# Kernel tuning notes

Hardware: AMD Instinct MI355X
Metric: run time of the kernel (lower is better)

Reference implementation:

```python
import jax, jax.numpy as jnp
import numpy as np

_EPSILON = 1e-06
EPS = 0.05
MAX_ITER = 50
THRESHOLD = 0.001


def setup_inputs() -> dict:
    key = jax.random.key(0)
    k1, k2 = jax.random.split(key)
    source = jax.random.normal(k1, (8192, 64), dtype=jnp.float32)
    target = jax.random.normal(k2, (8192, 64), dtype=jnp.float32)
    return {"source": source, "target": target}


def _sinkhorn(source, target):
    source = source.astype(jnp.float32)
    target = target.astype(jnp.float32)
    # squared euclidean cost matrix [N, M] (cdist(p=2)**2)
    sq_s = jnp.sum(source * source, axis=1, keepdims=True)          # [N,1]
    sq_t = jnp.sum(target * target, axis=1, keepdims=True).T        # [1,M]
    cost = sq_s + sq_t - 2.0 * (source @ target.T)                  # [N,M]
    cost = jnp.maximum(cost, 0.0)

    n_source, n_target = cost.shape
    log_mu = jnp.full((n_source,), jnp.log(jnp.maximum(1.0 / n_source, _EPSILON)), dtype=jnp.float32)
    log_nu = jnp.full((n_target,), jnp.log(jnp.maximum(1.0 / n_target, _EPSILON)), dtype=jnp.float32)

    u0 = jnp.zeros((n_source,), dtype=jnp.float32)
    v0 = jnp.zeros((n_target,), dtype=jnp.float32)

    def step(carry, _):
        u, v, done = carry
        prev_u = u
        mc = (-cost + u[:, None] + v[None, :]) / EPS
        u_new = EPS * (log_mu - jax.nn.logsumexp(mc, axis=1)) + u
        mc2 = (-cost + u_new[:, None] + v[None, :]) / EPS
        v_new = EPS * (log_nu - jax.nn.logsumexp(mc2, axis=0)) + v
        # freeze state once converged (emulates the torch early break)
        u = jnp.where(done, u, u_new)
        v = jnp.where(done, v, v_new)
        done = done | (jnp.mean(jnp.abs(u_new - prev_u)) < THRESHOLD)
        return (u, v, done), None

    (u, v, _), _ = jax.lax.scan(step, (u0, v0, jnp.array(False)), None, length=MAX_ITER)

    transport_plan = jnp.exp((-cost + u[:, None] + v[None, :]) / EPS)
    return jnp.sum(transport_plan * cost)


def reference(source, target):
    return _sinkhorn(source, target)
```

## Files before the change

kernel.cpp:

```cpp
#include <hip/hip_runtime.h>

#define N      8192
#define KDIM   64
#define SCALE2     28.853900817779268f
#define INV_SCALE2 0.034657359027997264f
#define TWOSCALE   57.707801635558536f
#define EPSLN2     0.034657359027997264f
#define EPS_LOG_MU (-0.45054566736396444f)
#define THRESH     0.001f
#define NEG_BIG    (-1e30f)
#define NCHUNK  32
#define COLSPAN 256
#define NCT     16
#define NBUF    5
#define ROWS_PER_BLOCK 256

typedef __attribute__((ext_vector_type(8))) short bf16x8;
typedef __attribute__((ext_vector_type(4))) float f32x4;

static __device__ __forceinline__ float exp2fast(float x) { return __builtin_amdgcn_exp2f(x); }
static __device__ __forceinline__ float log2fast(float x) { return __builtin_amdgcn_logf(x); }

static __device__ __forceinline__ unsigned short f2bf(float f) {
    unsigned u = __float_as_uint(f);
    u += 0x7FFFu + ((u >> 16) & 1u);
    return (unsigned short)(u >> 16);
}
static __device__ __forceinline__ float bf2f(unsigned short h) {
    return __uint_as_float(((unsigned)h) << 16);
}

static __device__ __forceinline__ void load16_to_lds(const void* gptr, void* lptr) {
    __builtin_amdgcn_global_load_lds(
        (const __attribute__((address_space(1))) unsigned int*)gptr,
        (__attribute__((address_space(3))) unsigned int*)lptr,
        16, 0, 0);
}

static __device__ __forceinline__ void stage_tile(
        const unsigned short* __restrict__ CPhi, const unsigned short* __restrict__ CPlo,
        char* ldsbuf, int jb, int wave, int swz) {
    const char* gsrc = (const char*)(wave < 2 ? CPhi : CPlo);
    const char* g = gsrc + (size_t)jb * 128 + (size_t)((wave & 1) * 1024 + swz);
    char* l = ldsbuf + (wave & 1) * 1024 + (wave >> 1) * 2048;
    load16_to_lds(g, l);
}

static __device__ __forceinline__ void load_held(
        const unsigned short* __restrict__ RPhi, const unsigned short* __restrict__ RPlo,
        int rowbase, int lrow, int kgrp, bf16x8 (&bh)[4][2], bf16x8 (&bl)[4][2]) {
#pragma unroll
    for (int it = 0; it < 4; ++it)
#pragma unroll
        for (int ks = 0; ks < 2; ++ks) {
            int boff = (rowbase + it * 16 + lrow) * KDIM + ks * 32 + kgrp * 8;
            bh[it][ks] = *reinterpret_cast<const bf16x8*>(RPhi + boff);
            bl[it][ks] = *reinterpret_cast<const bf16x8*>(RPlo + boff);
            asm volatile("" : "+v"(bh[it][ks]));
            asm volatile("" : "+v"(bl[it][ks]));
        }
}

static __device__ __forceinline__ void barrier_lds_only() {
    asm volatile("s_waitcnt lgkmcnt(0)" ::: "memory");
    __builtin_amdgcn_sched_barrier(0);
    __builtin_amdgcn_s_barrier();
    __builtin_amdgcn_sched_barrier(0);
}

static __device__ __forceinline__ void pipe_wait(int n) {
    if (n >= 3)      asm volatile("s_waitcnt vmcnt(3)" ::: "memory");
    else if (n == 2) asm volatile("s_waitcnt vmcnt(2)" ::: "memory");
    else if (n == 1) asm volatile("s_waitcnt vmcnt(1)" ::: "memory");
    else             asm volatile("s_waitcnt vmcnt(0)" ::: "memory");
    __builtin_amdgcn_sched_barrier(0);
    __builtin_amdgcn_s_barrier();
    __builtin_amdgcn_sched_barrier(0);
}

static __device__ __forceinline__ void lse_loop(
        const unsigned short* __restrict__ CPhi, const unsigned short* __restrict__ CPlo,
        char* ldsA, const float* lds_alpha,
        const bf16x8 (&bh)[4][2], const bf16x8 (&bl)[4][2],
        int jbase0, int wave, int lane, int swz, float (&m)[4], float (&s)[4]) {
    const int lrow = lane & 15, kgrp = lane >> 4;
    const int ro = lrow * 128;
    const int x0 = ((kgrp)     ^ (lrow & 7)) * 16;
    const int x1 = ((kgrp + 4) ^ (lrow & 7)) * 16;
#pragma unroll
    for (int ct = 0; ct < NCT; ++ct) {
        int w = NCT - 1 - ct; if (w > 3) w = 3;
        pipe_wait(w);
        if (ct + 4 < NCT)
            stage_tile(CPhi, CPlo, ldsA + ((ct + 4) % NBUF) * 4096,
                       jbase0 + (ct + 4) * 16, wave, swz);

        float4 av = *reinterpret_cast<const float4*>(lds_alpha + ct * 16 + kgrp * 4);
        const char* base = ldsA + (ct % NBUF) * 4096;
        bf16x8 ah0 = *reinterpret_cast<const bf16x8*>(base + ro + x0);
        bf16x8 ah1 = *reinterpret_cast<const bf16x8*>(base + ro + x1);
        bf16x8 al0 = *reinterpret_cast<const bf16x8*>(base + 2048 + ro + x0);
        bf16x8 al1 = *reinterpret_cast<const bf16x8*>(base + 2048 + ro + x1);

        __builtin_amdgcn_s_setprio(1);
        f32x4 acc[4];
#pragma unroll
        for (int it = 0; it < 4; ++it) {
            f32x4 a = {0.0f, 0.0f, 0.0f, 0.0f};
            a = __builtin_amdgcn_mfma_f32_16x16x32_bf16(ah0, bh[it][0], a, 0, 0, 0);
            a = __builtin_amdgcn_mfma_f32_16x16x32_bf16(ah1, bh[it][1], a, 0, 0, 0);
            a = __builtin_amdgcn_mfma_f32_16x16x32_bf16(al0, bh[it][0], a, 0, 0, 0);
            a = __builtin_amdgcn_mfma_f32_16x16x32_bf16(al1, bh[it][1], a, 0, 0, 0);
            a = __builtin_amdgcn_mfma_f32_16x16x32_bf16(ah0, bl[it][0], a, 0, 0, 0);
            a = __builtin_amdgcn_mfma_f32_16x16x32_bf16(ah1, bl[it][1], a, 0, 0, 0);
            acc[it] = a;
        }
        __builtin_amdgcn_s_setprio(0);

#pragma unroll
        for (int it = 0; it < 4; ++it) {
            float L0 = fmaf(TWOSCALE, acc[it][0], av.x);
            float L1 = fmaf(TWOSCALE, acc[it][1], av.y);
            float L2 = fmaf(TWOSCALE, acc[it][2], av.z);
            float L3 = fmaf(TWOSCALE, acc[it][3], av.w);
            float mx = fmaxf(fmaxf(L0, L1), fmaxf(L2, L3));
            float mn = fmaxf(m[it], mx);
            float rs = exp2fast(m[it] - mn);
            float e  = (exp2fast(L0 - mn) + exp2fast(L1 - mn)) +
                       (exp2fast(L2 - mn) + exp2fast(L3 - mn));
            s[it] = fmaf(s[it], rs, e);
            m[it] = mn;
        }
    }
}

static __device__ __forceinline__ void write_partials(
        float (&m)[4], float (&s)[4], float* __restrict__ pm, float* __restrict__ ps,
        const float* __restrict__ sqr2, int ck, int rowbase, int lane) {
    const int lrow = lane & 15, kgrp = lane >> 4;
#pragma unroll
    for (int off = 16; off < 64; off <<= 1) {
#pragma unroll
        for (int it = 0; it < 4; ++it) {
            float mo = __shfl_xor(m[it], off);
            float so = __shfl_xor(s[it], off);
            float mn = fmaxf(m[it], mo);
            s[it] = s[it] * exp2fast(m[it] - mn) + so * exp2fast(mo - mn);
            m[it] = mn;
        }
    }
    if (kgrp == 0) {
#pragma unroll
        for (int it = 0; it < 4; ++it) {
            int row = rowbase + it * 16 + lrow;
            pm[(size_t)ck * N + row] = m[it] - sqr2[row];
            ps[(size_t)ck * N + row] = s[it];
        }
    }
}

__global__ void norms_kernel(const float* __restrict__ S, const float* __restrict__ T,
                             float* __restrict__ sq_s2, float* __restrict__ sq_t2) {
    int t = blockIdx.x * blockDim.x + threadIdx.x;
    const float* p = (t < N) ? S : T;
    int r = t & (N - 1);
    const float4* row = reinterpret_cast<const float4*>(p + (size_t)r * KDIM);
    float acc = 0.0f;
#pragma unroll
    for (int q = 0; q < KDIM / 4; ++q) {
        float4 a = row[q];
        acc += a.x * a.x + a.y * a.y + a.z * a.z + a.w * a.w;
    }
    if (t < N) sq_s2[r] = acc * SCALE2; else sq_t2[r] = acc * SCALE2;
}

__global__ void init_kernel(float* u, float* v, float* alphaT,
                            const float* __restrict__ sq_t2, int* doneArr) {
    int t = blockIdx.x * blockDim.x + threadIdx.x;
    if (t < N) { u[t] = 0.0f; v[t] = 0.0f; alphaT[t] = -sq_t2[t]; }
    if (t == 0) { doneArr[0] = 0; doneArr[1] = 0; }
}

__global__ void split_kernel(const float* __restrict__ S, const float* __restrict__ T,
                             unsigned short* __restrict__ Shi, unsigned short* __restrict__ Slo,
                             unsigned short* __restrict__ Thi, unsigned short* __restrict__ Tlo) {
    int t = blockIdx.x * 256 + threadIdx.x;
    const int half = (N * KDIM) / 4;
    const float* src = (t < half) ? S : T;
    unsigned short* dhi = (t < half) ? Shi : Thi;
    unsigned short* dlo = (t < half) ? Slo : Tlo;
    int e = (t < half) ? t : t - half;
    float4 x = reinterpret_cast<const float4*>(src)[e];
    unsigned short h0 = f2bf(x.x), h1 = f2bf(x.y), h2 = f2bf(x.z), h3 = f2bf(x.w);
    ushort4 hv = make_ushort4(h0, h1, h2, h3);
    ushort4 lv = make_ushort4(f2bf(x.x - bf2f(h0)), f2bf(x.y - bf2f(h1)),
                              f2bf(x.z - bf2f(h2)), f2bf(x.w - bf2f(h3)));
    reinterpret_cast<ushort4*>(dhi)[e] = hv;
    reinterpret_cast<ushort4*>(dlo)[e] = lv;
}

__global__ __launch_bounds__(256, 4) void row_lse(
        const unsigned short* __restrict__ CPhi, const unsigned short* __restrict__ CPlo,
        const unsigned short* __restrict__ RPhi, const unsigned short* __restrict__ RPlo,
        const float* __restrict__ alphaG, const float* __restrict__ sqr2,
        float* __restrict__ pm, float* __restrict__ ps,
        const int* __restrict__ done) {
    if (*done) return;
    __shared__ __align__(16) char ldsA[NBUF * 4096];
    __shared__ __align__(16) float lds_alpha[COLSPAN];
    const int wave = threadIdx.x >> 6, lane = threadIdx.x & 63;
    const int lrow = lane & 15, kgrp = lane >> 4;
    const int ck = blockIdx.x & 31, rb = blockIdx.x >> 5;
    const int rowbase = rb * ROWS_PER_BLOCK + wave * 64;
    const int jbase0 = ck * COLSPAN;
    const int swz = (lane >> 3) * 128 + (((lane & 7) ^ ((lane >> 3) & 7)) << 4);

#pragma unroll
    for (int t = 0; t < 4; ++t)
        stage_tile(CPhi, CPlo, ldsA + t * 4096, jbase0 + t * 16, wave, swz);
    lds_alpha[threadIdx.x] = alphaG[jbase0 + threadIdx.x];

    bf16x8 bh[4][2], bl[4][2];
    load_held(RPhi, RPlo, rowbase, lrow, kgrp, bh, bl);

    float m[4] = {NEG_BIG, NEG_BIG, NEG_BIG, NEG_BIG};
    float s[4] = {0.0f, 0.0f, 0.0f, 0.0f};
    barrier_lds_only();

    lse_loop(CPhi, CPlo, ldsA, lds_alpha, bh, bl, jbase0, wave, lane, swz, m, s);
    write_partials(m, s, pm, ps, sqr2, ck, rowbase, lane);
}

__global__ __launch_bounds__(256, 4) void col_lse(
        const unsigned short* __restrict__ CPhi, const unsigned short* __restrict__ CPlo,
        const unsigned short* __restrict__ RPhi, const unsigned short* __restrict__ RPlo,
        const float* __restrict__ pm_in, const float* __restrict__ ps_in,
        const float* __restrict__ sqs2,
        float* __restrict__ u,
        float* __restrict__ blockDiff,
        const float* __restrict__ sqr2,
        float* __restrict__ pm, float* __restrict__ ps,
        const int* __restrict__ done) {
    if (*done) return;
    __shared__ __align__(16) char ldsA[NBUF * 4096];
    __shared__ __align__(16) float lds_alpha[COLSPAN];
    __shared__ float wsum[4];
    const int wave = threadIdx.x >> 6, lane = threadIdx.x & 63;
    const int lrow = lane & 15, kgrp = lane >> 4;
    const int ck = blockIdx.x & 31, rb = blockIdx.x >> 5;
    const int rowbase = rb * ROWS_PER_BLOCK + wave * 64;
    const int jbase0 = ck * COLSPAN;
    const int swz = (lane >> 3) * 128 + (((lane & 7) ^ ((lane >> 3) & 7)) << 4);

#pragma unroll
    for (int t = 0; t < 4; ++t)
        stage_tile(CPhi, CPlo, ldsA + t * 4096, jbase0 + t * 16, wave, swz);

    {
        int j = jbase0 + threadIdx.x;
        float mm = NEG_BIG, ss = 0.0f;
#pragma unroll
        for (int c = 0; c < NCHUNK; ++c) {
            float mc = pm_in[(size_t)c * N + j];
            float sc = ps_in[(size_t)c * N + j];
            float mn = fmaxf(mm, mc);
            ss = ss * exp2fast(mm - mn) + sc * exp2fast(mc - mn);
            mm = mn;
        }
        float unew = EPS_LOG_MU - EPSLN2 * (mm + log2fast(ss));
        lds_alpha[threadIdx.x] = fmaf(unew, SCALE2, -sqs2[j]);
        if (rb == 0) {
            float d = fabsf(unew - u[j]);
            u[j] = unew;
#pragma unroll
            for (int off = 32; off; off >>= 1) d += __shfl_xor(d, off);
            if (lane == 0) wsum[wave] = d;
        }
    }

    bf16x8 bh[4][2], bl[4][2];
    load_held(RPhi, RPlo, rowbase, lrow, kgrp, bh, bl);

    float m[4] = {NEG_BIG, NEG_BIG, NEG_BIG, NEG_BIG};
    float s[4] = {0.0f, 0.0f, 0.0f, 0.0f};
    barrier_lds_only();
    if (rb == 0 && threadIdx.x == 0)
        blockDiff[ck] = wsum[0] + wsum[1] + wsum[2] + wsum[3];

    lse_loop(CPhi, CPlo, ldsA, lds_alpha, bh, bl, jbase0, wave, lane, swz, m, s);
    write_partials(m, s, pm, ps, sqr2, ck, rowbase, lane);
}

__global__ __launch_bounds__(256) void v_reduce(const float* __restrict__ pm,
                                                const float* __restrict__ ps,
                                                float* __restrict__ v,
                                                float* __restrict__ alphaT,
                                                const float* __restrict__ sqt2,
                                                const float* __restrict__ blockDiff,
                                                const int* __restrict__ dcur,
                                                int* __restrict__ dnext) {
    if (*dcur) {
        if (blockIdx.x == 0 && threadIdx.x == 0) *dnext = 1;
        return;
    }
    int j = blockIdx.x * 256 + threadIdx.x;
    float m = NEG_BIG, s = 0.0f;
#pragma unroll
    for (int c = 0; c < NCHUNK; ++c) {
        float mc = pm[(size_t)c * N + j];
        float sc = ps[(size_t)c * N + j];
        float mn = fmaxf(m, mc);
        s = s * exp2fast(m - mn) + sc * exp2fast(mc - mn);
        m = mn;
    }
    float vnew = EPS_LOG_MU - EPSLN2 * (m + log2fast(s));
    v[j] = vnew;
    alphaT[j] = fmaf(vnew, SCALE2, -sqt2[j]);

    if (blockIdx.x == 0 && threadIdx.x < 64) {
        float sum = (threadIdx.x < 32) ? blockDiff[threadIdx.x] : 0.0f;
#pragma unroll
        for (int off = 32; off; off >>= 1) sum += __shfl_xor(sum, off);
        if (threadIdx.x == 0)
            *dnext = (sum * (1.0f / (float)N) < THRESH) ? 1 : 0;
    }
}

__global__ __launch_bounds__(256, 4) void plan_mfma(
        const unsigned short* __restrict__ CPhi, const unsigned short* __restrict__ CPlo,
        const unsigned short* __restrict__ RPhi, const unsigned short* __restrict__ RPlo,
        const float* __restrict__ u, const float* __restrict__ v,
        const float* __restrict__ sqr2, const float* __restrict__ sqc2,
        float* __restrict__ part) {
    __shared__ __align__(16) char ldsA[NBUF * 4096];
    __shared__ __align__(16) float lds_v2[COLSPAN];
    __shared__ __align__(16) float lds_sqc[COLSPAN];
    __shared__ float wsum[4];
    const int wave = threadIdx.x >> 6, lane = threadIdx.x & 63;
    const int lrow = lane & 15, kgrp = lane >> 4;
    const int ck = blockIdx.x & 31, rb = blockIdx.x >> 5;
    const int rowbase = rb * ROWS_PER_BLOCK + wave * 64;
    const int jbase0 = ck * COLSPAN;
    const int swz = (lane >> 3) * 128 + (((lane & 7) ^ ((lane >> 3) & 7)) << 4);

#pragma unroll
    for (int t = 0; t < 4; ++t)
        stage_tile(CPhi, CPlo, ldsA + t * 4096, jbase0 + t * 16, wave, swz);
    lds_v2[threadIdx.x]  = v[jbase0 + threadIdx.x] * SCALE2;
    lds_sqc[threadIdx.x] = sqc2[jbase0 + threadIdx.x];

    bf16x8 bh[4][2], bl[4][2];
    load_held(RPhi, RPlo, rowbase, lrow, kgrp, bh, bl);

    float sqr_i[4], u2_i[4];
#pragma unroll
    for (int it = 0; it < 4; ++it) {
        int row = rowbase + it * 16 + lrow;
        sqr_i[it] = sqr2[row];
        u2_i[it]  = u[row] * SCALE2;
    }

    float lsum = 0.0f;
    barrier_lds_only();

    const int ro = lrow * 128;
    const int x0 = ((kgrp)     ^ (lrow & 7)) * 16;
    const int x1 = ((kgrp + 4) ^ (lrow & 7)) * 16;
#pragma unroll
    for (int ct = 0; ct < NCT; ++ct) {
        int w = NCT - 1 - ct; if (w > 3) w = 3;
        pipe_wait(w);
        if (ct + 4 < NCT)
            stage_tile(CPhi, CPlo, ldsA + ((ct + 4) % NBUF) * 4096,
                       jbase0 + (ct + 4) * 16, wave, swz);

        float4 v2 = *reinterpret_cast<const float4*>(lds_v2 + ct * 16 + kgrp * 4);
        float4 sc = *reinterpret_cast<const float4*>(lds_sqc + ct * 16 + kgrp * 4);
        const char* base = ldsA + (ct % NBUF) * 4096;
        bf16x8 ah0 = *reinterpret_cast<const bf16x8*>(base + ro + x0);
        bf16x8 ah1 = *reinterpret_cast<const bf16x8*>(base + ro + x1);
        bf16x8 al0 = *reinterpret_cast<const bf16x8*>(base + 2048 + ro + x0);
        bf16x8 al1 = *reinterpret_cast<const bf16x8*>(base + 2048 + ro + x1);

        __builtin_amdgcn_s_setprio(1);
        f32x4 acc[4];
#pragma unroll
        for (int it = 0; it < 4; ++it) {
            f32x4 a = {0.0f, 0.0f, 0.0f, 0.0f};
            a = __builtin_amdgcn_mfma_f32_16x16x32_bf16(ah0, bh[it][0], a, 0, 0, 0);
            a = __builtin_amdgcn_mfma_f32_16x16x32_bf16(ah1, bh[it][1], a, 0, 0, 0);
            a = __builtin_amdgcn_mfma_f32_16x16x32_bf16(al0, bh[it][0], a, 0, 0, 0);
            a = __builtin_amdgcn_mfma_f32_16x16x32_bf16(al1, bh[it][1], a, 0, 0, 0);
            a = __builtin_amdgcn_mfma_f32_16x16x32_bf16(ah0, bl[it][0], a, 0, 0, 0);
            a = __builtin_amdgcn_mfma_f32_16x16x32_bf16(ah1, bl[it][1], a, 0, 0, 0);
            acc[it] = a;
        }
        __builtin_amdgcn_s_setprio(0);

        float vs[4] = {v2.x, v2.y, v2.z, v2.w};
        float ss[4] = {sc.x, sc.y, sc.z, sc.w};
#pragma unroll
        for (int it = 0; it < 4; ++it) {
#pragma unroll
            for (int r = 0; r < 4; ++r) {
                float c2 = fmaxf(sqr_i[it] + ss[r] - TWOSCALE * acc[it][r], 0.0f);
                lsum = fmaf(exp2fast(u2_i[it] + vs[r] - c2), c2, lsum);
            }
        }
    }
    lsum *= INV_SCALE2;

#pragma unroll
    for (int off = 32; off; off >>= 1) lsum += __shfl_xor(lsum, off);
    if (lane == 0) wsum[wave] = lsum;
    __syncthreads();
    if (threadIdx.x == 0)
        part[blockIdx.x] = wsum[0] + wsum[1] + wsum[2] + wsum[3];
}

__global__ void final_reduce(const float* __restrict__ part, float* __restrict__ out) {
    int t = threadIdx.x;
    float sum = 0.0f;
    for (int i = t; i < 1024; i += 256) sum += part[i];
#pragma unroll
    for (int off = 32; off; off >>= 1) sum += __shfl_xor(sum, off);
    __shared__ float wsum[4];
    int lane = t & 63, wave = t >> 6;
    if (lane == 0) wsum[wave] = sum;
    __syncthreads();
    if (t == 0) out[0] = wsum[0] + wsum[1] + wsum[2] + wsum[3];
}

extern "C" void kernel_launch(void* const* d_in, const int* in_sizes, int n_in,
                              void* d_out, int out_size, void* d_ws, size_t ws_size,
                              hipStream_t stream) {
    const float* S = (const float*)d_in[0];
    const float* T = (const float*)d_in[1];
    float* out = (float*)d_out;

    unsigned short* us = (unsigned short*)d_ws;
    unsigned short* Shi = us;
    unsigned short* Slo = us + (size_t)N * KDIM;
    unsigned short* Thi = us + (size_t)2 * N * KDIM;
    unsigned short* Tlo = us + (size_t)3 * N * KDIM;
    float* w = (float*)(us + (size_t)4 * N * KDIM);
    size_t off = 0;
    float* sq_s2     = w + off; off += N;
    float* sq_t2     = w + off; off += N;
    float* u         = w + off; off += N;
    float* v         = w + off; off += N;
    float* alphaT    = w + off; off += N;
    float* pmA       = w + off; off += (size_t)NCHUNK * N;
    float* psA       = w + off; off += (size_t)NCHUNK * N;
    float* pmB       = w + off; off += (size_t)NCHUNK * N;
    float* psB       = w + off; off += (size_t)NCHUNK * N;
    float* blockDiff = w + off; off += 64;
    float* part      = w + off; off += 1024;
    int*   doneArr   = (int*)(w + off);

    hipLaunchKernelGGL(norms_kernel, dim3(64),   dim3(256), 0, stream, S, T, sq_s2, sq_t2);
    hipLaunchKernelGGL(init_kernel,  dim3(32),   dim3(256), 0, stream, u, v, alphaT, sq_t2, doneArr);
    hipLaunchKernelGGL(split_kernel, dim3(1024), dim3(256), 0, stream, S, T, Shi, Slo, Thi, Tlo);

    const int LSE_BLOCKS = (N / ROWS_PER_BLOCK) * NCHUNK;
    for (int it = 0; it < 50; ++it) {
        int* dcur  = doneArr + (it & 1);
        int* dnext = doneArr + ((it + 1) & 1);
        hipLaunchKernelGGL(row_lse, dim3(LSE_BLOCKS), dim3(256), 0, stream,
                           Thi, Tlo, Shi, Slo, alphaT, sq_s2, pmA, psA, dcur);
        hipLaunchKernelGGL(col_lse, dim3(LSE_BLOCKS), dim3(256), 0, stream,
                           Shi, Slo, Thi, Tlo, pmA, psA, sq_s2, u, blockDiff,
                           sq_t2, pmB, psB, dcur);
        hipLaunchKernelGGL(v_reduce, dim3(32), dim3(256), 0, stream,
                           pmB, psB, v, alphaT, sq_t2, blockDiff, dcur, dnext);
    }

    hipLaunchKernelGGL(plan_mfma, dim3(LSE_BLOCKS), dim3(256), 0, stream,
                       Thi, Tlo, Shi, Slo, u, v, sq_s2, sq_t2, part);
    hipLaunchKernelGGL(final_reduce, dim3(1), dim3(256), 0, stream, part, out);
}
```

Before: 3.370 ms.

## Fuse v-reduction into row_lse prologue and drop per-iteration v_reduce launch

```diff
diff --git a/kernel.cpp b/kernel.cpp
--- a/kernel.cpp
+++ b/kernel.cpp
@@ -159,6 +159,13 @@
     }
 }
 
+static __device__ __forceinline__ bool conv_done(const float* __restrict__ bd) {
+    float sd = 0.0f;
+#pragma unroll
+    for (int c = 0; c < 32; ++c) sd += bd[c];
+    return sd * (1.0f / (float)N) < THRESH;
+}
+
 __global__ void norms_kernel(const float* __restrict__ S, const float* __restrict__ T,
                              float* __restrict__ sq_s2, float* __restrict__ sq_t2) {
     int t = blockIdx.x * blockDim.x + threadIdx.x;
@@ -174,11 +181,10 @@
     if (t < N) sq_s2[r] = acc * SCALE2; else sq_t2[r] = acc * SCALE2;
 }
 
-__global__ void init_kernel(float* u, float* v, float* alphaT,
-                            const float* __restrict__ sq_t2, int* doneArr) {
+__global__ void init_kernel(float* u, float* v, float* blockDiff) {
     int t = blockIdx.x * blockDim.x + threadIdx.x;
-    if (t < N) { u[t] = 0.0f; v[t] = 0.0f; alphaT[t] = -sq_t2[t]; }
-    if (t == 0) { doneArr[0] = 0; doneArr[1] = 0; }
+    if (t < N) { u[t] = 0.0f; v[t] = 0.0f; }
+    if (t < 128) blockDiff[t] = 1.0e9f;
 }
 
 __global__ void split_kernel(const float* __restrict__ S, const float* __restrict__ T,
@@ -202,10 +208,12 @@
 __global__ __launch_bounds__(256, 4) void row_lse(
         const unsigned short* __restrict__ CPhi, const unsigned short* __restrict__ CPlo,
         const unsigned short* __restrict__ RPhi, const unsigned short* __restrict__ RPlo,
-        const float* __restrict__ alphaG, const float* __restrict__ sqr2,
+        const float* __restrict__ pmV, const float* __restrict__ psV,
+        const float* __restrict__ sqc2,
+        const float* __restrict__ sqr2,
         float* __restrict__ pm, float* __restrict__ ps,
-        const int* __restrict__ done) {
-    if (*done) return;
+        const float* __restrict__ bdPrev, int first) {
+    if (!first && conv_done(bdPrev)) return;
     __shared__ __align__(16) char ldsA[NBUF * 4096];
     __shared__ __align__(16) float lds_alpha[COLSPAN];
     const int wave = threadIdx.x >> 6, lane = threadIdx.x & 63;
@@ -218,7 +226,27 @@
 #pragma unroll
     for (int t = 0; t < 4; ++t)
         stage_tile(CPhi, CPlo, ldsA + t * 4096, jbase0 + t * 16, wave, swz);
-    lds_alpha[threadIdx.x] = alphaG[jbase0 + threadIdx.x];
+
+    {
+        int j = jbase0 + threadIdx.x;
+        float a;
+        if (first) {
+            a = -sqc2[j];
+        } else {
+            float mm = NEG_BIG, ss = 0.0f;
+#pragma unroll
+            for (int c = 0; c < NCHUNK; ++c) {
+                float mc = pmV[(size_t)c * N + j];
+                float sc = psV[(size_t)c * N + j];
+                float mn = fmaxf(mm, mc);
+                ss = ss * exp2fast(mm - mn) + sc * exp2fast(mc - mn);
+                mm = mn;
+            }
+            float vnew = EPS_LOG_MU - EPSLN2 * (mm + log2fast(ss));
+            a = fmaf(vnew, SCALE2, -sqc2[j]);
+        }
+        lds_alpha[threadIdx.x] = a;
+    }
 
     bf16x8 bh[4][2], bl[4][2];
     load_held(RPhi, RPlo, rowbase, lrow, kgrp, bh, bl);
@@ -237,17 +265,20 @@
         const float* __restrict__ pm_in, const float* __restrict__ ps_in,
         const float* __restrict__ sqs2,
         float* __restrict__ u,
-        float* __restrict__ blockDiff,
+        const float* __restrict__ bdPrev,
+        float* __restrict__ bdCur,
         const float* __restrict__ sqr2,
-        float* __restrict__ pm, float* __restrict__ ps,
-        const int* __restrict__ done) {
-    if (*done) return;
+        float* __restrict__ pm, float* __restrict__ ps) {
+    const int ck = blockIdx.x & 31, rb = blockIdx.x >> 5;
+    if (conv_done(bdPrev)) {
+        if (rb == 0 && threadIdx.x == 0) bdCur[ck] = 0.0f;
+        return;
+    }
     __shared__ __align__(16) char ldsA[NBUF * 4096];
     __shared__ __align__(16) float lds_alpha[COLSPAN];
     __shared__ float wsum[4];
     const int wave = threadIdx.x >> 6, lane = threadIdx.x & 63;
     const int lrow = lane & 15, kgrp = lane >> 4;
-    const int ck = blockIdx.x & 31, rb = blockIdx.x >> 5;
     const int rowbase = rb * ROWS_PER_BLOCK + wave * 64;
     const int jbase0 = ck * COLSPAN;
     const int swz = (lane >> 3) * 128 + (((lane & 7) ^ ((lane >> 3) & 7)) << 4);
@@ -285,24 +316,15 @@
     float s[4] = {0.0f, 0.0f, 0.0f, 0.0f};
     barrier_lds_only();
     if (rb == 0 && threadIdx.x == 0)
-        blockDiff[ck] = wsum[0] + wsum[1] + wsum[2] + wsum[3];
+        bdCur[ck] = wsum[0] + wsum[1] + wsum[2] + wsum[3];
 
     lse_loop(CPhi, CPlo, ldsA, lds_alpha, bh, bl, jbase0, wave, lane, swz, m, s);
     write_partials(m, s, pm, ps, sqr2, ck, rowbase, lane);
 }
 
-__global__ __launch_bounds__(256) void v_reduce(const float* __restrict__ pm,
-                                                const float* __restrict__ ps,
-                                                float* __restrict__ v,
-                                                float* __restrict__ alphaT,
-                                                const float* __restrict__ sqt2,
-                                                const float* __restrict__ blockDiff,
-                                                const int* __restrict__ dcur,
-                                                int* __restrict__ dnext) {
-    if (*dcur) {
-        if (blockIdx.x == 0 && threadIdx.x == 0) *dnext = 1;
-        return;
-    }
+__global__ __launch_bounds__(256) void v_final(const float* __restrict__ pm,
+                                               const float* __restrict__ ps,
+                                               float* __restrict__ v) {
     int j = blockIdx.x * 256 + threadIdx.x;
     float m = NEG_BIG, s = 0.0f;
 #pragma unroll
@@ -313,17 +335,7 @@
         s = s * exp2fast(m - mn) + sc * exp2fast(mc - mn);
         m = mn;
     }
-    float vnew = EPS_LOG_MU - EPSLN2 * (m + log2fast(s));
-    v[j] = vnew;
-    alphaT[j] = fmaf(vnew, SCALE2, -sqt2[j]);
-
-    if (blockIdx.x == 0 && threadIdx.x < 64) {
-        float sum = (threadIdx.x < 32) ? blockDiff[threadIdx.x] : 0.0f;
-#pragma unroll
-        for (int off = 32; off; off >>= 1) sum += __shfl_xor(sum, off);
-        if (threadIdx.x == 0)
-            *dnext = (sum * (1.0f / (float)N) < THRESH) ? 1 : 0;
-    }
+    v[j] = EPS_LOG_MU - EPSLN2 * (m + log2fast(s));
 }
 
 __global__ __launch_bounds__(256, 4) void plan_mfma(
@@ -449,32 +461,30 @@
     float* sq_t2     = w + off; off += N;
     float* u         = w + off; off += N;
     float* v         = w + off; off += N;
-    float* alphaT    = w + off; off += N;
     float* pmA       = w + off; off += (size_t)NCHUNK * N;
     float* psA       = w + off; off += (size_t)NCHUNK * N;
     float* pmB       = w + off; off += (size_t)NCHUNK * N;
     float* psB       = w + off; off += (size_t)NCHUNK * N;
-    float* blockDiff = w + off; off += 64;
+    float* blockDiff = w + off; off += 128;
     float* part      = w + off; off += 1024;
-    int*   doneArr   = (int*)(w + off);
 
     hipLaunchKernelGGL(norms_kernel, dim3(64),   dim3(256), 0, stream, S, T, sq_s2, sq_t2);
-    hipLaunchKernelGGL(init_kernel,  dim3(32),   dim3(256), 0, stream, u, v, alphaT, sq_t2, doneArr);
+    hipLaunchKernelGGL(init_kernel,  dim3(32),   dim3(256), 0, stream, u, v, blockDiff);
     hipLaunchKernelGGL(split_kernel, dim3(1024), dim3(256), 0, stream, S, T, Shi, Slo, Thi, Tlo);
 
     const int LSE_BLOCKS = (N / ROWS_PER_BLOCK) * NCHUNK;
     for (int it = 0; it < 50; ++it) {
-        int* dcur  = doneArr + (it & 1);
-        int* dnext = doneArr + ((it + 1) & 1);
+        float* bdPrev = blockDiff + ((it + 1) & 1) * 64;
+        float* bdCur  = blockDiff + (it & 1) * 64;
         hipLaunchKernelGGL(row_lse, dim3(LSE_BLOCKS), dim3(256), 0, stream,
-                           Thi, Tlo, Shi, Slo, alphaT, sq_s2, pmA, psA, dcur);
+                           Thi, Tlo, Shi, Slo, pmB, psB, sq_t2, sq_s2,
+                           pmA, psA, bdPrev, it == 0 ? 1 : 0);
         hipLaunchKernelGGL(col_lse, dim3(LSE_BLOCKS), dim3(256), 0, stream,
-                           Shi, Slo, Thi, Tlo, pmA, psA, sq_s2, u, blockDiff,
-                           sq_t2, pmB, psB, dcur);
-        hipLaunchKernelGGL(v_reduce, dim3(32), dim3(256), 0, stream,
-                           pmB, psB, v, alphaT, sq_t2, blockDiff, dcur, dnext);
-    }
-
+                           Shi, Slo, Thi, Tlo, pmA, psA, sq_s2, u,
+                           bdPrev, bdCur, sq_t2, pmB, psB);
+    }
+
+    hipLaunchKernelGGL(v_final, dim3(32), dim3(256), 0, stream, pmB, psB, v);
     hipLaunchKernelGGL(plan_mfma, dim3(LSE_BLOCKS), dim3(256), 0, stream,
                        Thi, Tlo, Shi, Slo, u, v, sq_s2, sq_t2, part);
     hipLaunchKernelGGL(final_reduce, dim3(1), dim3(256), 0, stream, part, out);
```

Measured after the change: 3.277 ms, median of 2. 1.03x faster.
